# Kernel optimization log

Hardware: AMD Instinct MI355X
Metric: run time of the kernel (lower is better)

## Reference

```python
import jax, jax.numpy as jnp
import numpy as np

NUM_GROUPS = 32
EPS = 1e-6


def group_norm(x, gamma, beta):
    # x: [B, C, H, W]; GroupNorm over (C//G, H, W) per group, affine per-channel
    B, C, H, W = x.shape
    xg = x.reshape(B, NUM_GROUPS, C // NUM_GROUPS, H, W)
    mean = xg.mean(axis=(2, 3, 4), keepdims=True)
    var = ((xg - mean) ** 2).mean(axis=(2, 3, 4), keepdims=True)
    xg = (xg - mean) * jax.lax.rsqrt(var + EPS)
    x = xg.reshape(B, C, H, W)
    return x * gamma[None, :, None, None] + beta[None, :, None, None]


def setup_inputs() -> dict:
    key = jax.random.key(0)
    ks = jax.random.split(key, 8)
    n, t, c, h, w = 2, 16, 64, 64, 64
    M = 512  # memory-bank slots
    inv_sqrt_c = 1.0 / np.sqrt(c).astype(np.float32)
    return {
        "x": jax.random.normal(ks[0], (n, t, c, h, w), jnp.float32),
        "gn_gamma": 1.0 + 0.1 * jax.random.normal(ks[1], (c,), jnp.float32),
        "gn_beta": 0.1 * jax.random.normal(ks[2], (c,), jnp.float32),
        "phi_w": jax.random.normal(ks[3], (c, c), jnp.float32) * inv_sqrt_c,
        "phi_b": 0.01 * jax.random.normal(ks[4], (c,), jnp.float32),
        "mb": jax.random.normal(ks[5], (c, M), jnp.float32),
        "wz_w": jax.random.normal(ks[6], (c, c), jnp.float32) * inv_sqrt_c,
        "wz_b": 0.01 * jax.random.normal(ks[7], (c,), jnp.float32),
    }


def reference(x, gn_gamma, gn_beta, phi_w, phi_b, mb, wz_w, wz_b):
    # Faithful MMA forward, batched across all t frames at once (the torch
    # code loops per-frame; math is identical frame-wise).
    n, t, c, h, w = x.shape
    xb = x.reshape(n * t, c, h, w)
    q_ = group_norm(xb, gn_gamma, gn_beta)
    # 1x1 conv == per-pixel channel matmul
    phi = jnp.einsum('oc,bchw->bohw', phi_w, q_) + phi_b[None, :, None, None]
    phi = phi.reshape(n * t, c, h * w).transpose(0, 2, 1)  # [B, HW, C]
    scale = jnp.asarray(c, phi.dtype) ** -0.5
    f1 = jnp.einsum('bpc,cm->bpm', phi, mb) * scale          # [B, HW, 512]
    attn = jax.nn.softmax(f1, axis=-1)
    y1 = jnp.einsum('bpm,cm->bpc', attn, mb)                 # [B, HW, C]
    y1 = y1.transpose(0, 2, 1).reshape(n * t, c, h, w)
    wy = jnp.einsum('oc,bchw->bohw', wz_w, y1) + wz_b[None, :, None, None]
    out = wy + xb  # residual with the (pre-norm) frame, as in torch
    return out.reshape(n, t, c, h, w)
```

## Files before the change

### kernel.cpp

```cpp
#include <hip/hip_runtime.h>
#include <hip/hip_bf16.h>

#define NFRAME 32
#define CCH 64
#define HW 4096
#define MSLOT 512

typedef __attribute__((ext_vector_type(8))) short s16x8;
typedef __attribute__((ext_vector_type(16))) float f32x16;
typedef __attribute__((ext_vector_type(4))) unsigned int u32x4;
typedef __attribute__((ext_vector_type(2))) unsigned int u32x2;
typedef unsigned short u16;
typedef unsigned int u32;

#define WS_STATS 0
#define WS_OFF   2048
#define WS_BF16  4096
#define BW_KF    0
#define BW_VF    32768
#define BW_WZF   65536
#define BW_WFF   69632

#define QSCALE 0.18033688011112042f

static __device__ __forceinline__ u16 f2b(float f) {
  __hip_bfloat16 h = __float2bfloat16(f);
  return *reinterpret_cast<u16*>(&h);
}
static __device__ __forceinline__ u32 pack2(float a, float b) {
  u32 r;
  asm("v_cvt_pk_bf16_f32 %0, %1, %2" : "=v"(r) : "v"(a), "v"(b));
  return r;
}
static __device__ __forceinline__ f32x16 zero16() {
  f32x16 z;
#pragma unroll
  for (int r = 0; r < 16; ++r) z[r] = 0.f;
  return z;
}
static __device__ __forceinline__ void d2b(const float* e, s16x8& f0, s16x8& f1) {
#pragma unroll
  for (int mh = 0; mh < 2; ++mh) {
    const u32 P0 = pack2(e[mh * 8 + 0], e[mh * 8 + 1]);
    const u32 P1 = pack2(e[mh * 8 + 2], e[mh * 8 + 3]);
    const u32 Q0 = pack2(e[mh * 8 + 4], e[mh * 8 + 5]);
    const u32 Q1 = pack2(e[mh * 8 + 6], e[mh * 8 + 7]);
    const u32x2 s0 = __builtin_amdgcn_permlane32_swap(P0, Q0, false, false);
    const u32x2 s1 = __builtin_amdgcn_permlane32_swap(P1, Q1, false, false);
    u32x4 bw = {s0[0], s1[0], s0[1], s1[1]};
    if (mh == 0) f0 = __builtin_bit_cast(s16x8, bw);
    else         f1 = __builtin_bit_cast(s16x8, bw);
  }
}

__global__ __launch_bounds__(256) void k_pre(const float* __restrict__ x,
                                             const float* __restrict__ mb,
                                             const float* __restrict__ wz_w,
                                             float* __restrict__ ws) {
  if (blockIdx.x < 1024) {
    const int bg = blockIdx.x;
    const float4* xp = (const float4*)(x + (size_t)bg * 8192);
    const int t = threadIdx.x;
    float s = 0.f, s2 = 0.f;
#pragma unroll
    for (int i = 0; i < 8; ++i) {
      float4 v = xp[t + i * 256];
      s  += v.x + v.y + v.z + v.w;
      s2 += v.x * v.x + v.y * v.y + v.z * v.z + v.w * v.w;
    }
    for (int off = 32; off; off >>= 1) {
      s  += __shfl_down(s,  off, 64);
      s2 += __shfl_down(s2, off, 64);
    }
    __shared__ float ls[8];
    const int wid = t >> 6;
    if ((t & 63) == 0) { ls[wid * 2] = s; ls[wid * 2 + 1] = s2; }
    __syncthreads();
    if (t == 0) {
      float S = 0.f, S2 = 0.f;
#pragma unroll
      for (int w = 0; w < 4; ++w) { S += ls[w * 2]; S2 += ls[w * 2 + 1]; }
      float mean = S * (1.f / 8192.f);
      float var  = S2 * (1.f / 8192.f) - mean * mean;
      float rstd = rsqrtf(var + 1e-6f);
      ws[WS_STATS + bg * 2]     = mean;
      ws[WS_STATS + bg * 2 + 1] = rstd;
    }
    return;
  }
  u16* wbw = (u16*)(ws + WS_BF16);
  const int i = (blockIdx.x - 1024) * 256 + threadIdx.x;
  if (i < 32768) {
    const int j = i & 7, l = (i >> 3) & 63, ks = (i >> 9) & 3, q = i >> 11;
    const int c = ks * 16 + ((l >> 5) << 3) + j;
    const int m = q * 32 + (l & 31);
    wbw[BW_KF + i] = f2b(mb[c * MSLOT + m]);
  } else if (i < 65536) {
    const int i2 = i - 32768;
    const int j = i2 & 7, l = (i2 >> 3) & 63, ct = (i2 >> 9) & 1, mh = (i2 >> 10) & 1, q = i2 >> 11;
    const int c = ct * 32 + (l & 31);
    const int m = q * 32 + mh * 16 + ((l >> 5) << 3) + j;
    wbw[BW_VF + i2] = f2b(mb[c * MSLOT + m]);
  } else {
    const int i3 = i - 65536;
    const int j = i3 & 7, l = (i3 >> 3) & 63, ks = (i3 >> 9) & 3, ot = i3 >> 11;
    const int o = ot * 32 + (l & 31);
    const int c = ks * 16 + ((l >> 5) << 3) + j;
    wbw[BW_WZF + i3] = f2b(wz_w[o * 64 + c]);
  }
}

__global__ __launch_bounds__(256) void k_prep(const float* __restrict__ phi_w,
                                              const float* __restrict__ phi_b,
                                              const float* __restrict__ gamma,
                                              const float* __restrict__ beta,
                                              float* __restrict__ ws) {
  const int b = blockIdx.x;
  const int o = threadIdx.x & 63;
  const int quad = threadIdx.x >> 6;
  __shared__ u16 wrow[64 * 64];
  __shared__ float offp[256];
  float offacc = 0.f;
#pragma unroll
  for (int ci = 0; ci < 16; ++ci) {
    const int c = quad * 16 + ci;
    const int g = c >> 1;
    const float mean = ws[WS_STATS + (b * 32 + g) * 2];
    const float rstd = ws[WS_STATS + (b * 32 + g) * 2 + 1];
    const float a = gamma[c] * rstd;
    const float d = beta[c] - mean * a;
    const float wv = phi_w[o * 64 + c];
    wrow[o * 64 + c] = f2b(wv * a * QSCALE);
    offacc += wv * d;
  }
  offp[threadIdx.x] = offacc;
  __syncthreads();
  if (quad == 0) {
    const float off = offp[o] + offp[64 + o] + offp[128 + o] + offp[192 + o];
    ws[WS_OFF + b * 64 + o] = (off + phi_b[o]) * QSCALE;
  }
  u16* wff = (u16*)(ws + WS_BF16) + BW_WFF + (size_t)b * 4096;
#pragma unroll
  for (int k = 0; k < 16; ++k) {
    const int il = threadIdx.x * 16 + k;
    const int j = il & 7, l = (il >> 3) & 63, ks = (il >> 9) & 3, ot = il >> 11;
    const int oo = ot * 32 + (l & 31);
    const int c = ks * 16 + ((l >> 5) << 3) + j;
    wff[il] = wrow[oo * 64 + c];
  }
}

__global__ __launch_bounds__(256, 2) void k_main(const float* __restrict__ x,
                                                 const float* __restrict__ ws,
                                                 const float* __restrict__ wz_b,
                                                 float* __restrict__ out) {
  const int b    = blockIdx.x >> 4;
  const int tile = blockIdx.x & 15;
  const int w    = threadIdx.x >> 6;
  const int lane = threadIdx.x & 63;
  const int l5 = lane & 31;
  const int hi = lane >> 5;
  const int pbase = tile * 256 + w * 64 + l5;

  const u16* wb = (const u16*)(ws + WS_BF16);
  const float* xb = x + (size_t)b * CCH * HW;

  s16x8 q[2][4];
#pragma unroll
  for (int pt = 0; pt < 2; ++pt) {
    const int p = pbase + pt * 32;
    s16x8 bx[4];
#pragma unroll
    for (int ks = 0; ks < 4; ++ks) {
      const float* xc = xb + (size_t)(ks * 16 + hi * 8) * HW + p;
      float v[8];
#pragma unroll
      for (int j = 0; j < 8; ++j) v[j] = xc[(size_t)j * HW];
      u32x4 pk = {pack2(v[0], v[1]), pack2(v[2], v[3]),
                  pack2(v[4], v[5]), pack2(v[6], v[7])};
      bx[ks] = __builtin_bit_cast(s16x8, pk);
    }
    const float* offb = ws + WS_OFF + b * 64;
#pragma unroll
    for (int ot = 0; ot < 2; ++ot) {
      f32x16 acc = zero16();
#pragma unroll
      for (int ks = 0; ks < 4; ++ks) {
        const s16x8 a = *(const s16x8*)(wb + BW_WFF + ((((size_t)b * 2 + ot) * 4 + ks) * 64 + lane) * 8);
        acc = __builtin_amdgcn_mfma_f32_32x32x16_bf16(a, bx[ks], acc, 0, 0, 0);
      }
      float e[16];
#pragma unroll
      for (int rq = 0; rq < 4; ++rq) {
        const float4 offv = *(const float4*)(offb + ot * 32 + rq * 8 + hi * 4);
#pragma unroll
        for (int rr = 0; rr < 4; ++rr) e[rq * 4 + rr] = acc[rq * 4 + rr] + ((const float*)&offv)[rr];
      }
      d2b(e, q[pt][ot * 2], q[pt][ot * 2 + 1]);
    }
  }

  f32x16 Y[2][2];
#pragma unroll
  for (int pt = 0; pt < 2; ++pt)
#pragma unroll
    for (int ct = 0; ct < 2; ++ct) Y[pt][ct] = zero16();
  float Lacc[2] = {0.f, 0.f};

#pragma unroll 2
  for (int mt = 0; mt < 16; ++mt) {
    s16x8 kf[4], vf[4];
#pragma unroll
    for (int ks = 0; ks < 4; ++ks)
      kf[ks] = *(const s16x8*)(wb + BW_KF + (((size_t)mt * 4 + ks) * 64 + lane) * 8);
#pragma unroll
    for (int i = 0; i < 4; ++i)
      vf[i] = *(const s16x8*)(wb + BW_VF + (((size_t)mt * 4 + i) * 64 + lane) * 8);

#pragma unroll
    for (int pt = 0; pt < 2; ++pt) {
      f32x16 s = zero16();
#pragma unroll
      for (int ks = 0; ks < 4; ++ks)
        s = __builtin_amdgcn_mfma_f32_32x32x16_bf16(kf[ks], q[pt][ks], s, 0, 0, 0);
      float e[16];
      float ls = 0.f;
#pragma unroll
      for (int r = 0; r < 16; ++r) { e[r] = exp2f(s[r]); ls += e[r]; }
      Lacc[pt] += ls;
      s16x8 pf0, pf1;
      d2b(e, pf0, pf1);
#pragma unroll
      for (int ct = 0; ct < 2; ++ct) {
        Y[pt][ct] = __builtin_amdgcn_mfma_f32_32x32x16_bf16(vf[ct],     pf0, Y[pt][ct], 0, 0, 0);
        Y[pt][ct] = __builtin_amdgcn_mfma_f32_32x32x16_bf16(vf[2 + ct], pf1, Y[pt][ct], 0, 0, 0);
      }
    }
  }

#pragma unroll
  for (int pt = 0; pt < 2; ++pt) {
    const int p = pbase + pt * 32;
    const float Ltot = Lacc[pt] + __shfl_xor(Lacc[pt], 32, 64);
    const float invL = 1.f / Ltot;
    s16x8 by[4];
#pragma unroll
    for (int ct = 0; ct < 2; ++ct) {
      float e[16];
#pragma unroll
      for (int r = 0; r < 16; ++r) e[r] = Y[pt][ct][r] * invL;
      d2b(e, by[ct * 2], by[ct * 2 + 1]);
    }
    const float* xr = xb + p;
    float* ob = out + (size_t)b * CCH * HW + p;
#pragma unroll
    for (int ot = 0; ot < 2; ++ot) {
      f32x16 acc = zero16();
#pragma unroll
      for (int ks = 0; ks < 4; ++ks) {
        const s16x8 a = *(const s16x8*)(wb + BW_WZF + (((size_t)ot * 4 + ks) * 64 + lane) * 8);
        acc = __builtin_amdgcn_mfma_f32_32x32x16_bf16(a, by[ks], acc, 0, 0, 0);
      }
#pragma unroll
      for (int rq = 0; rq < 4; ++rq) {
        const int obase = ot * 32 + rq * 8 + hi * 4;
        const float4 bz = *(const float4*)(wz_b + obase);
#pragma unroll
        for (int rr = 0; rr < 4; ++rr) {
          const size_t idx = (size_t)(obase + rr) * HW;
          ob[idx] = acc[rq * 4 + rr] + ((const float*)&bz)[rr] + xr[idx];
        }
      }
    }
  }
}

extern "C" void kernel_launch(void* const* d_in, const int* in_sizes, int n_in,
                              void* d_out, int out_size, void* d_ws, size_t ws_size,
                              hipStream_t stream) {
  const float* x     = (const float*)d_in[0];
  const float* gamma = (const float*)d_in[1];
  const float* beta  = (const float*)d_in[2];
  const float* phi_w = (const float*)d_in[3];
  const float* phi_b = (const float*)d_in[4];
  const float* mb    = (const float*)d_in[5];
  const float* wz_w  = (const float*)d_in[6];
  const float* wz_b  = (const float*)d_in[7];
  float* out = (float*)d_out;
  float* ws  = (float*)d_ws;

  k_pre<<<1296, 256, 0, stream>>>(x, mb, wz_w, ws);
  k_prep<<<32, 256, 0, stream>>>(phi_w, phi_b, gamma, beta, ws);
  k_main<<<NFRAME * 16, 256, 0, stream>>>(x, ws, wz_b, out);
}
```

Measured before the change: 51.93 us.

## Stage memory-bank K/V fragments through LDS with double-buffered async loads

Interleaves the bf16 K and V fragments of the memory bank into a per-slot-tile layout. Each block then cooperatively prefetches the next tile into a double-buffered LDS area with global_load_lds, instead of every wave reading the same fragments from global/L2. This cuts redundant global traffic and overlaps loading with MFMA work. The cost is a block-wide barrier per iteration and 16KB of LDS per block, which could limit occupancy or stall waves.

```diff
diff --git a/kernel.cpp b/kernel.cpp
--- a/kernel.cpp
+++ b/kernel.cpp
@@ -16,8 +16,7 @@
 #define WS_STATS 0
 #define WS_OFF   2048
 #define WS_BF16  4096
-#define BW_KF    0
-#define BW_VF    32768
+#define BW_KV    0
 #define BW_WZF   65536
 #define BW_WFF   69632
 
@@ -90,17 +89,20 @@
   }
   u16* wbw = (u16*)(ws + WS_BF16);
   const int i = (blockIdx.x - 1024) * 256 + threadIdx.x;
-  if (i < 32768) {
-    const int j = i & 7, l = (i >> 3) & 63, ks = (i >> 9) & 3, q = i >> 11;
-    const int c = ks * 16 + ((l >> 5) << 3) + j;
-    const int m = q * 32 + (l & 31);
-    wbw[BW_KF + i] = f2b(mb[c * MSLOT + m]);
-  } else if (i < 65536) {
-    const int i2 = i - 32768;
-    const int j = i2 & 7, l = (i2 >> 3) & 63, ct = (i2 >> 9) & 1, mh = (i2 >> 10) & 1, q = i2 >> 11;
-    const int c = ct * 32 + (l & 31);
-    const int m = q * 32 + mh * 16 + ((l >> 5) << 3) + j;
-    wbw[BW_VF + i2] = f2b(mb[c * MSLOT + m]);
+  if (i < 65536) {
+    const int j = i & 7, l = (i >> 3) & 63, f = (i >> 9) & 7, mt = i >> 12;
+    float v;
+    if (f < 4) {
+      const int c = f * 16 + ((l >> 5) << 3) + j;
+      const int m = mt * 32 + (l & 31);
+      v = mb[c * MSLOT + m];
+    } else {
+      const int idx = f - 4;
+      const int c = (idx & 1) * 32 + (l & 31);
+      const int m = mt * 32 + (idx >> 1) * 16 + ((l >> 5) << 3) + j;
+      v = mb[c * MSLOT + m];
+    }
+    wbw[BW_KV + i] = f2b(v);
   } else {
     const int i3 = i - 65536;
     const int j = i3 & 7, l = (i3 >> 3) & 63, ks = (i3 >> 9) & 3, ot = i3 >> 11;
@@ -165,6 +167,22 @@
   const u16* wb = (const u16*)(ws + WS_BF16);
   const float* xb = x + (size_t)b * CCH * HW;
 
+  __shared__ __align__(16) u16 kv[2][8][512];
+
+#define STAGE(mt_, nb_)                                                          \
+  {                                                                              \
+    _Pragma("unroll")                                                            \
+    for (int k = 0; k < 2; ++k) {                                                \
+      const int f = w * 2 + k;                                                   \
+      const u16* src = wb + BW_KV + ((size_t)(mt_) * 8 + f) * 512 + lane * 8;    \
+      __builtin_amdgcn_global_load_lds(                                          \
+          (const __attribute__((address_space(1))) void*)src,                    \
+          (__attribute__((address_space(3))) void*)&kv[nb_][f][0], 16, 0, 0);    \
+    }                                                                            \
+  }
+
+  STAGE(0, 0);
+
   s16x8 q[2][4];
 #pragma unroll
   for (int pt = 0; pt < 2; ++pt) {
@@ -207,15 +225,20 @@
     for (int ct = 0; ct < 2; ++ct) Y[pt][ct] = zero16();
   float Lacc[2] = {0.f, 0.f};
 
+  __syncthreads();
+
 #pragma unroll 2
   for (int mt = 0; mt < 16; ++mt) {
+    const int cb = mt & 1;
+    if (mt < 15) STAGE(mt + 1, cb ^ 1);
+
     s16x8 kf[4], vf[4];
 #pragma unroll
     for (int ks = 0; ks < 4; ++ks)
-      kf[ks] = *(const s16x8*)(wb + BW_KF + (((size_t)mt * 4 + ks) * 64 + lane) * 8);
+      kf[ks] = *(const s16x8*)&kv[cb][ks][(size_t)lane * 8];
 #pragma unroll
     for (int i = 0; i < 4; ++i)
-      vf[i] = *(const s16x8*)(wb + BW_VF + (((size_t)mt * 4 + i) * 64 + lane) * 8);
+      vf[i] = *(const s16x8*)&kv[cb][4 + i][(size_t)lane * 8];
 
 #pragma unroll
     for (int pt = 0; pt < 2; ++pt) {
@@ -236,6 +259,7 @@
         Y[pt][ct] = __builtin_amdgcn_mfma_f32_32x32x16_bf16(vf[2 + ct], pf1, Y[pt][ct], 0, 0, 0);
       }
     }
+    __syncthreads();
   }
 
 #pragma unroll
@@ -273,6 +297,7 @@
       }
     }
   }
+#undef STAGE
 }
 
 extern "C" void kernel_launch(void* const* d_in, const int* in_sizes, int n_in,
```

Result: faster. 50.39 us (-3.0%).
